# Optimization experiments

Measured on AMD Instinct MI355X. Metric: run time of the kernel, lower is better.

## Reference

```python
import jax, jax.numpy as jnp
import numpy as np

EPS = 1e-7
PROJ_EPS = 1e-5
MAX_TANH_ARG = 15.0
COMBINE_RELS_WEIGHT = 0.1


def _norm(x):
    return jnp.sqrt(jnp.sum(x * x, axis=-1, keepdims=True))


def log_map_zero(x):
    n = _norm(x)
    nc = jnp.clip(n, EPS, 1.0 - PROJ_EPS)
    return jnp.arctanh(nc) * x / jnp.maximum(n, EPS)


def exp_map_zero(v):
    n = jnp.maximum(_norm(v), EPS)
    return jnp.tanh(jnp.minimum(n, MAX_TANH_ARG)) * v / n


def hyperbolic_projection(x):
    n = jnp.maximum(_norm(x), EPS)
    maxnorm = 1.0 - PROJ_EPS
    return x * jnp.minimum(1.0, maxnorm / n)


def mobius_addition(u, v):
    uv = jnp.sum(u * v, axis=-1, keepdims=True)
    u2 = jnp.sum(u * u, axis=-1, keepdims=True)
    v2 = jnp.sum(v * v, axis=-1, keepdims=True)
    num = (1.0 + 2.0 * uv + v2) * u + (1.0 - u2) * v
    den = 1.0 + 2.0 * uv + u2 * v2
    return num / jnp.maximum(den, EPS)


def setup_inputs() -> dict:
    key = jax.random.key(0)
    ks = jax.random.split(key, 9)
    N, R, D, E = 50000, 1000, 128, 640000
    # embeddings start well inside the Poincare ball
    ents = 0.01 * jax.random.normal(ks[0], (N, D), dtype=jnp.float32)
    rels = 0.01 * jax.random.normal(ks[1], (R, D), dtype=jnp.float32)
    W_ent = jax.random.normal(ks[2], (D, D), dtype=jnp.float32) * (1.0 / np.sqrt(D))
    bias_vec = jnp.zeros((1, D), dtype=jnp.float32)
    ent_row = jax.random.randint(ks[3], (E,), 0, N, dtype=jnp.int32)
    ent_col = jax.random.randint(ks[4], (E,), 0, N, dtype=jnp.int32)
    rel_row = jax.random.randint(ks[5], (E,), 0, N, dtype=jnp.int32)
    rel_val = jax.random.randint(ks[6], (E,), 0, R, dtype=jnp.int32)
    near_rels_num = (1.0 + jax.random.randint(ks[7], (N,), 0, 32, dtype=jnp.int32)).astype(jnp.float32)
    return {"ents_embed_input": ents, "rels_embed_input": rels, "W_ent": W_ent,
            "bias_vec": bias_vec, "ent_row": ent_row, "ent_col": ent_col,
            "rel_row": rel_row, "rel_val": rel_val, "near_rels_num": near_rels_num}


def reference(ents_embed_input, rels_embed_input, W_ent, bias_vec,
              ent_row, ent_col, rel_row, rel_val, near_rels_num):
    N = ents_embed_input.shape[0]
    # tangent-space map + linear transform
    ents_tan = log_map_zero(ents_embed_input)          # [N, D]
    h = ents_tan @ W_ent                                # [N, D]
    # GAT-style sparse attention on adjacency (scores are detached in original)
    hd = jax.lax.stop_gradient(h)
    scores = jnp.sum(hd[ent_row] * hd[ent_col], axis=-1)  # [E]
    m = jax.ops.segment_max(scores, ent_row, num_segments=N)
    e = jnp.exp(scores - m[ent_row])
    denom = jax.ops.segment_sum(e, ent_row, num_segments=N)
    alpha = e / jnp.maximum(denom[ent_row], EPS)           # [E]
    near_ents = jax.ops.segment_sum(alpha[:, None] * h[ent_col], ent_row, num_segments=N)
    # relation neighborhood mean (gather + scatter-sum)
    edge_emb = rels_embed_input[rel_val]                   # [E, D]
    near_rels = jax.ops.segment_sum(edge_emb, rel_row, num_segments=N)
    near_rels = near_rels / near_rels_num[:, None]
    out = hyperbolic_projection(exp_map_zero(near_ents + COMBINE_RELS_WEIGHT * near_rels))
    b = hyperbolic_projection(exp_map_zero(bias_vec))
    out = hyperbolic_projection(mobius_addition(out, b))
    return out
```

## Files before the change

kernel.cpp:

```cpp
#include <hip/hip_runtime.h>
#include <hip/hip_fp16.h>
#include <math.h>

#define EPS 1e-7f
#define PROJ_EPS 1e-5f
#define MAXNORM (1.0f - PROJ_EPS)
#define D_DIM 128
#define CAP 48
#define PSHIFT 7
#define NPART 392
#define PCAP 2048
#define CHUNK 4096
#define NCONV 32
#define ATS 136
#define WTS 136
#define PREP_SMEM (64 * 132 * 4)
#define MID_SMEM (64 * ATS * 2 + 128 * WTS * 2 + 256)

typedef _Float16 f16;
typedef __attribute__((ext_vector_type(4))) _Float16 f16x4;
typedef __attribute__((ext_vector_type(8))) _Float16 f16x8;
typedef __attribute__((ext_vector_type(4))) float f32x4;

__device__ inline float wred(float v) {
    #pragma unroll
    for (int o = 32; o; o >>= 1) v += __shfl_xor(v, o, 64);
    return v;
}
__device__ inline float gred(float v) {
    v += __shfl_xor(v, 1, 64);
    v += __shfl_xor(v, 2, 64);
    v += __shfl_xor(v, 4, 64);
    v += __shfl_xor(v, 8, 64);
    return v;
}
__device__ inline void gred2(float& a, float& b) {
    a += __shfl_xor(a, 1, 64);  b += __shfl_xor(b, 1, 64);
    a += __shfl_xor(a, 2, 64);  b += __shfl_xor(b, 2, 64);
    a += __shfl_xor(a, 4, 64);  b += __shfl_xor(b, 4, 64);
    a += __shfl_xor(a, 8, 64);  b += __shfl_xor(b, 8, 64);
}
__device__ inline __half2 bc_h2(unsigned int u) { return *(__half2*)&u; }
__device__ inline unsigned int bc_u32(__half2 h) { return *(unsigned int*)&h; }

typedef _Float16 h2v __attribute__((ext_vector_type(2)));
__device__ inline h2v as_h2v(unsigned int u) { union { unsigned int u; h2v h; } c; c.u = u; return c.h; }

__device__ inline float dot8d(uint4 a, uint4 v) {
#if __has_builtin(__builtin_amdgcn_fdot2)
    float s = __builtin_amdgcn_fdot2(as_h2v(a.x), as_h2v(v.x), 0.f, false);
    s = __builtin_amdgcn_fdot2(as_h2v(a.y), as_h2v(v.y), s, false);
    s = __builtin_amdgcn_fdot2(as_h2v(a.z), as_h2v(v.z), s, false);
    s = __builtin_amdgcn_fdot2(as_h2v(a.w), as_h2v(v.w), s, false);
    return s;
#else
    __half2 t = __hmul2(bc_h2(a.x), bc_h2(v.x));
    t = __hfma2(bc_h2(a.y), bc_h2(v.y), t);
    t = __hfma2(bc_h2(a.z), bc_h2(v.z), t);
    t = __hfma2(bc_h2(a.w), bc_h2(v.w), t);
    return __low2float(t) + __high2float(t);
#endif
}
__device__ inline void acc8h(__half2* A, float w, uint4 v) {
    __half2 w2 = __float2half2_rn(w);
    A[0] = __hfma2(w2, bc_h2(v.x), A[0]);
    A[1] = __hfma2(w2, bc_h2(v.y), A[1]);
    A[2] = __hfma2(w2, bc_h2(v.z), A[2]);
    A[3] = __hfma2(w2, bc_h2(v.w), A[3]);
}
__device__ inline void add8h(__half2* A, uint4 v) {
    A[0] = __hadd2(A[0], bc_h2(v.x));
    A[1] = __hadd2(A[1], bc_h2(v.y));
    A[2] = __hadd2(A[2], bc_h2(v.z));
    A[3] = __hadd2(A[3], bc_h2(v.w));
}

__global__ __launch_bounds__(256) void k_prep(
    const float* __restrict__ W, f16* __restrict__ Wt_h,
    const int* __restrict__ er, const int* __restrict__ ec,
    const int* __restrict__ rr, const int* __restrict__ rv,
    int* __restrict__ part_e, int* __restrict__ part_r,
    int* __restrict__ cursors,
    const float* __restrict__ bias, float* __restrict__ bws,
    const float* __restrict__ rels, f16* __restrict__ rels_h, int relsN4,
    int E, int nChunk) {
    __shared__ alignas(16) unsigned char smem[PREP_SMEM];
    int tid = threadIdx.x;
    int bid = blockIdx.x;

    if (bid == 0) {
        if (tid < 64) {
            int l = tid;
            float2 bv = ((const float2*)bias)[l];
            float bn = fmaxf(sqrtf(wred(bv.x * bv.x + bv.y * bv.y)), EPS);
            float gb = tanhf(fminf(bn, 15.f)) / bn;
            float bx = gb * bv.x, by = gb * bv.y;
            float nb = fmaxf(sqrtf(wred(bx * bx + by * by)), EPS);
            float pb = fminf(1.f, MAXNORM / nb);
            bx *= pb; by *= pb;
            ((float2*)bws)[l] = make_float2(bx, by);
            float v2 = wred(bx * bx + by * by);
            if (l == 0) bws[128] = v2;
        }
        return;
    }

    if (bid == 1) {
        float* lts = (float*)smem;
        unsigned int* wt_u = (unsigned int*)Wt_h;
        for (int pass = 0; pass < 2; pass++) {
            #pragma unroll
            for (int i = 0; i < 8; i++) {
                int flat = (tid + i * 256) * 4;
                int kr = flat >> 7, cc = flat & 127;
                float4 x = *(const float4*)(W + (size_t)(pass * 64 + kr) * D_DIM + cc);
                *(float4*)&lts[kr * 132 + cc] = x;
            }
            __syncthreads();
            #pragma unroll
            for (int i = 0; i < 16; i++) {
                int flat2 = tid + i * 256;
                int c = flat2 >> 5, kp = flat2 & 31;
                float lo = lts[(2 * kp) * 132 + c];
                float hi = lts[(2 * kp + 1) * 132 + c];
                wt_u[c * 64 + pass * 32 + kp] = bc_u32(__float22half2_rn(make_float2(lo, hi)));
            }
            __syncthreads();
        }
        return;
    }

    if (bid < 2 + NCONV) {
        int gtid = (bid - 2) * 256 + tid;
        for (int i = gtid; i < relsN4; i += NCONV * 256) {
            float4 x = ((const float4*)rels)[i];
            uint2 u;
            u.x = bc_u32(__float22half2_rn(make_float2(x.x, x.y)));
            u.y = bc_u32(__float22half2_rn(make_float2(x.z, x.w)));
            ((uint2*)rels_h)[i] = u;
        }
        return;
    }

    int pid = bid - 2 - NCONV;
    int pair = (pid >= nChunk) ? 1 : 0;
    int chunk = pair ? pid - nChunk : pid;
    int* hist = (int*)smem;
    int* dlt  = hist + NPART;
    int* sc   = dlt + NPART;
    int* st   = sc + 256;
    const int* rsrc = pair ? rr : er;
    const int* psrc = pair ? rv : ec;
    int* part = pair ? part_r : part_e;
    int* cur  = cursors + pair * NPART;
    int e0 = chunk * CHUNK;
    int n = min(CHUNK, E - e0);

    for (int i = tid; i < NPART; i += 256) hist[i] = 0;
    __syncthreads();

    int myr[16], rk[16];
    #pragma unroll
    for (int i = 0; i < 16; i++) {
        int e = e0 + tid + i * 256;
        if (e < E) {
            int r = rsrc[e];
            myr[i] = r;
            rk[i] = atomicAdd(&hist[r >> PSHIFT], 1);
        } else myr[i] = -1;
    }
    __syncthreads();

    int h0 = (2 * tid < NPART) ? hist[2 * tid] : 0;
    int h1 = (2 * tid + 1 < NPART) ? hist[2 * tid + 1] : 0;
    int s = h0 + h1;
    sc[tid] = s;
    __syncthreads();
    for (int off = 1; off < 256; off <<= 1) {
        int v = (tid >= off) ? sc[tid - off] : 0;
        __syncthreads();
        sc[tid] += v;
        __syncthreads();
    }
    int excl = sc[tid] - s;
    if (2 * tid < NPART) dlt[2 * tid] = excl;
    if (2 * tid + 1 < NPART) dlt[2 * tid + 1] = excl + h0;
    __syncthreads();

    #pragma unroll
    for (int i = 0; i < 16; i++) {
        if (myr[i] >= 0) {
            int e = e0 + tid + i * 256;
            unsigned int pk = ((unsigned int)myr[i] << 16) | (unsigned int)(psrc[e] & 0xFFFF);
            st[dlt[myr[i] >> PSHIFT] + rk[i]] = (int)pk;
        }
    }
    __syncthreads();

    for (int p = tid; p < NPART; p += 256) {
        int len = hist[p];
        if (len > 0) {
            int g = atomicAdd(&cur[p], len);
            if (g + len > PCAP) g = PCAP - len;
            if (g < 0) g = 0;
            dlt[p] = p * PCAP + g - dlt[p];
        }
    }
    __syncthreads();

    for (int i = tid; i < n; i += 256) {
        unsigned int v = (unsigned int)st[i];
        int p = (int)(v >> 16) >> PSHIFT;
        part[dlt[p] + i] = (int)v;
    }
}

__global__ __launch_bounds__(256) void k_mid(
    const float* __restrict__ ents, const f16* __restrict__ Wt_h,
    __half* __restrict__ hh,
    const int* __restrict__ part_e, const int* __restrict__ part_r,
    const int* __restrict__ cursors,
    unsigned short* __restrict__ pay_e, unsigned short* __restrict__ pay_r,
    int* __restrict__ cnt, int N, int nGemm) {
    __shared__ alignas(16) unsigned char smem[MID_SMEM];
    int tid = threadIdx.x;
    int bid = blockIdx.x;

    if (bid < nGemm) {
        f16* atile = (f16*)smem;
        f16* wtile = (f16*)(smem + 64 * ATS * 2);
        float* fac = (float*)(smem + 64 * ATS * 2 + 128 * WTS * 2);
        int lane = tid & 63;
        int wv = tid >> 6;
        int r0 = bid * 64;

        #pragma unroll
        for (int i = 0; i < 8; i++) {
            int flat = (tid + i * 256) * 4;
            int rr2 = flat >> 7, cc = flat & 127;
            float4 x = make_float4(0.f, 0.f, 0.f, 0.f);
            if (r0 + rr2 < N) x = *(const float4*)(ents + (size_t)(r0 + rr2) * D_DIM + cc);
            f16x4 v4 = {(f16)x.x, (f16)x.y, (f16)x.z, (f16)x.w};
            *(f16x4*)&atile[rr2 * ATS + cc] = v4;
            float s = x.x * x.x + x.y * x.y + x.z * x.z + x.w * x.w;
            s += __shfl_xor(s, 1, 64);
            s += __shfl_xor(s, 2, 64);
            s += __shfl_xor(s, 4, 64);
            s += __shfl_xor(s, 8, 64);
            s += __shfl_xor(s, 16, 64);
            if ((lane & 31) == 0) fac[rr2] = s;
        }
        #pragma unroll
        for (int i = 0; i < 8; i++) {
            int flat4 = tid + i * 256;
            int c = flat4 >> 4, off = (flat4 & 15) * 8;
            uint4 u = ((const uint4*)Wt_h)[flat4];
            *(uint4*)&wtile[c * WTS + off] = u;
        }
        __syncthreads();

        if (tid < 64) {
            float n = sqrtf(fac[tid]);
            float ncl = fminf(fmaxf(n, EPS), MAXNORM);
            float at = 0.5f * logf((1.f + ncl) / (1.f - ncl));
            fac[tid] = at / fmaxf(n, EPS);
        }
        __syncthreads();

        int l15 = lane & 15, kseg = lane >> 4;
        int arow = wv * 16 + l15;

        f32x4 acc[8];
        #pragma unroll
        for (int ct = 0; ct < 8; ct++) acc[ct] = (f32x4){0.f, 0.f, 0.f, 0.f};

        #pragma unroll
        for (int ks = 0; ks < 4; ks++) {
            int k0 = ks * 32 + kseg * 8;
            f16x8 af = *(const f16x8*)&atile[arow * ATS + k0];
            #pragma unroll
            for (int ct = 0; ct < 8; ct++) {
                f16x8 bf = *(const f16x8*)&wtile[(ct * 16 + l15) * WTS + k0];
                acc[ct] = __builtin_amdgcn_mfma_f32_16x16x32_f16(af, bf, acc[ct], 0, 0, 0);
            }
        }
        __syncthreads();

        #pragma unroll
        for (int rg = 0; rg < 4; rg++) {
            int m = wv * 16 + kseg * 4 + rg;
            float fc = fac[m];
            #pragma unroll
            for (int ct = 0; ct < 8; ct++) {
                atile[m * ATS + ct * 16 + l15] = (f16)(acc[ct][rg] * fc);
            }
        }
        __syncthreads();

        #pragma unroll
        for (int i = 0; i < 4; i++) {
            int flat4 = tid + i * 256;
            int rr2 = flat4 >> 4, off = (flat4 & 15) * 8;
            if (r0 + rr2 < N) {
                uint4 u = *(const uint4*)&atile[rr2 * ATS + off];
                *(uint4*)((char*)hh + ((size_t)(r0 + rr2)) * 256 + off * 2) = u;
            }
        }
        return;
    }

    int b2 = bid - nGemm;
    int pair = (b2 >= NPART) ? 1 : 0;
    int p = pair ? b2 - NPART : b2;
    int* bcnt = (int*)smem;
    unsigned short* bb = (unsigned short*)(smem + 512);
    const int* part = (pair ? part_r : part_e) + (size_t)p * PCAP;
    unsigned short* pay = pair ? pay_r : pay_e;
    int* cnt_out = cnt + (size_t)pair * N;
    int n = min(cursors[pair * NPART + p], PCAP);

    if (tid < 128) bcnt[tid] = 0;
    __syncthreads();

    for (int i = tid; i < n; i += 256) {
        unsigned int v = (unsigned int)part[i];
        int rl = (int)((v >> 16) & 127);
        int slot = atomicAdd(&bcnt[rl], 1);
        if (slot < CAP) bb[rl * CAP + slot] = (unsigned short)(v & 0xFFFF);
    }
    __syncthreads();

    int rbase = p * 128;
    uint4* gdst = (uint4*)(pay + (size_t)rbase * CAP);
    const uint4* gsrc = (const uint4*)bb;
    for (int i = tid; i < 768; i += 256) gdst[i] = gsrc[i];
    if (tid < 128 && rbase + tid < N) cnt_out[rbase + tid] = bcnt[tid];
}

__global__ __launch_bounds__(256) void k_row(
    const __half* __restrict__ hh, const __half* __restrict__ rels_h,
    const float* __restrict__ bws, const float* __restrict__ nrn,
    const int* __restrict__ cnt, const unsigned short* __restrict__ pay_e,
    const unsigned short* __restrict__ pay_r,
    float* __restrict__ out, int N) {
    int wv = threadIdx.x >> 6, lane = threadIdx.x & 63;
    int r = blockIdx.x * 4 + wv;
    if (r >= N) return;
    int sub = lane >> 4;
    int sl = lane & 15;

    const char* hB = (const char*)hh + sl * 16;
    const char* rB = (const char*)rels_h + sl * 16;
    uint4 hraw = *(const uint4*)(hB + ((size_t)r << 8));

    int deg  = min(cnt[r], CAP);
    int degr = min(cnt[N + r], CAP);
    int myidx = (lane < deg)  ? (int)pay_e[(size_t)r * CAP + lane] : 0;
    int myrel = (lane < degr) ? (int)pay_r[(size_t)r * CAP + lane] : 0;

    __half2 aA[4] = {bc_h2(0u), bc_h2(0u), bc_h2(0u), bc_h2(0u)};
    float den = 0.f;
    int full = deg >> 2, rem = deg & 3;
    int t = 0;
    for (; t + 2 <= full; t += 2) {
        int c0 = __shfl(myidx, t * 4 + sub);
        int c1 = __shfl(myidx, t * 4 + 4 + sub);
        uint4 v0 = *(const uint4*)(hB + ((size_t)c0 << 8));
        uint4 v1 = *(const uint4*)(hB + ((size_t)c1 << 8));
        float s0 = dot8d(hraw, v0);
        float s1 = dot8d(hraw, v1);
        gred2(s0, s1);
        float w0 = __expf(s0), w1 = __expf(s1);
        den += w0 + w1;
        acc8h(aA, w0, v0);
        acc8h(aA, w1, v1);
    }
    if (t < full) {
        int c0 = __shfl(myidx, t * 4 + sub);
        uint4 v0 = *(const uint4*)(hB + ((size_t)c0 << 8));
        float s0 = gred(dot8d(hraw, v0));
        float w0 = __expf(s0);
        den += w0;
        acc8h(aA, w0, v0);
    }
    if (rem) {
        int c0 = __shfl(myidx, full * 4 + sub);
        uint4 v0 = *(const uint4*)(hB + ((size_t)c0 << 8));
        float s0 = gred(dot8d(hraw, v0));
        float w0 = (sub < rem) ? __expf(s0) : 0.f;
        den += w0;
        acc8h(aA, w0, v0);
    }

    __half2 rA[4] = {bc_h2(0u), bc_h2(0u), bc_h2(0u), bc_h2(0u)};
    int fq = degr >> 2, rq = degr & 3;
    int q = 0;
    for (; q + 2 <= fq; q += 2) {
        int i0 = __shfl(myrel, q * 4 + sub);
        int i1 = __shfl(myrel, q * 4 + 4 + sub);
        uint4 v0 = *(const uint4*)(rB + ((size_t)i0 << 8));
        uint4 v1 = *(const uint4*)(rB + ((size_t)i1 << 8));
        add8h(rA, v0);
        add8h(rA, v1);
    }
    if (q < fq) {
        int i0 = __shfl(myrel, q * 4 + sub);
        uint4 v0 = *(const uint4*)(rB + ((size_t)i0 << 8));
        add8h(rA, v0);
    }
    if (rq) {
        int i0 = __shfl(myrel, fq * 4 + sub);
        uint4 v0 = *(const uint4*)(rB + ((size_t)i0 << 8));
        if (sub < rq) add8h(rA, v0);
    }

    den += __shfl_xor(den, 16, 64);
    den += __shfl_xor(den, 32, 64);
    #pragma unroll
    for (int st2 = 16; st2 <= 32; st2 <<= 1) {
        #pragma unroll
        for (int j = 0; j < 4; j++) {
            unsigned int ua = (unsigned int)__shfl_xor((int)bc_u32(aA[j]), st2, 64);
            aA[j] = __hadd2(aA[j], bc_h2(ua));
            unsigned int ur = (unsigned int)__shfl_xor((int)bc_u32(rA[j]), st2, 64);
            rA[j] = __hadd2(rA[j], bc_h2(ur));
        }
    }

    float inv  = 1.f / fmaxf(den, EPS);
    float innr = 0.1f / nrn[r];
    float2 a0 = __half22float2(aA[0]), a1 = __half22float2(aA[1]);
    float2 a2 = __half22float2(aA[2]), a3 = __half22float2(aA[3]);
    float2 r0f = __half22float2(rA[0]), r1f = __half22float2(rA[1]);
    float2 r2f = __half22float2(rA[2]), r3f = __half22float2(rA[3]);
    float v0 = a0.x * inv + r0f.x * innr, v1 = a0.y * inv + r0f.y * innr;
    float v2_ = a1.x * inv + r1f.x * innr, v3 = a1.y * inv + r1f.y * innr;
    float v4 = a2.x * inv + r2f.x * innr, v5 = a2.y * inv + r2f.y * innr;
    float v6 = a3.x * inv + r3f.x * innr, v7 = a3.y * inv + r3f.y * innr;

    float pn = v0*v0 + v1*v1 + v2_*v2_ + v3*v3 + v4*v4 + v5*v5 + v6*v6 + v7*v7;
    pn = gred(pn);
    float sq = sqrtf(pn);
    float nn = fmaxf(sq, EPS);
    float tt = __expf(2.f * fminf(nn, 15.f));
    float g = (tt - 1.f) / ((tt + 1.f) * nn);
    float n2 = fmaxf(g * sq, EPS);
    float pf = fminf(1.f, MAXNORM / n2);
    float gp = g * pf;
    float o0 = gp*v0, o1 = gp*v1, o2 = gp*v2_, o3 = gp*v3;
    float o4 = gp*v4, o5 = gp*v5, o6 = gp*v6, o7 = gp*v7;
    float un = n2 * pf;
    float u2 = un * un;

    const float4* bp = (const float4*)(bws + sl * 8);
    float4 b0 = bp[0], b1 = bp[1];
    float bv2 = bws[128];
    float puv = o0*b0.x + o1*b0.y + o2*b0.z + o3*b0.w
              + o4*b1.x + o5*b1.y + o6*b1.z + o7*b1.w;
    puv = gred(puv);
    float ca = 1.f + 2.f * puv + bv2;
    float cb = 1.f - u2;
    float idm = 1.f / fmaxf(1.f + 2.f * puv + u2 * bv2, EPS);
    float x0 = (ca*o0 + cb*b0.x) * idm, x1 = (ca*o1 + cb*b0.y) * idm;
    float x2 = (ca*o2 + cb*b0.z) * idm, x3 = (ca*o3 + cb*b0.w) * idm;
    float x4 = (ca*o4 + cb*b1.x) * idm, x5 = (ca*o5 + cb*b1.y) * idm;
    float x6 = (ca*o6 + cb*b1.z) * idm, x7 = (ca*o7 + cb*b1.w) * idm;
    float pr = x0*x0 + x1*x1 + x2*x2 + x3*x3 + x4*x4 + x5*x5 + x6*x6 + x7*x7;
    pr = gred(pr);
    float n3 = fmaxf(sqrtf(pr), EPS);
    float pf3 = fminf(1.f, MAXNORM / n3);

    if (sub == 0) {
        float4* op = (float4*)(out + (size_t)r * D_DIM + sl * 8);
        op[0] = make_float4(x0 * pf3, x1 * pf3, x2 * pf3, x3 * pf3);
        op[1] = make_float4(x4 * pf3, x5 * pf3, x6 * pf3, x7 * pf3);
    }
}

extern "C" void kernel_launch(void* const* d_in, const int* in_sizes, int n_in,
                              void* d_out, int out_size, void* d_ws, size_t ws_size,
                              hipStream_t stream) {
    const float* ents = (const float*)d_in[0];
    const float* rels = (const float*)d_in[1];
    const float* W    = (const float*)d_in[2];
    const float* bias = (const float*)d_in[3];
    const int* er = (const int*)d_in[4];
    const int* ec = (const int*)d_in[5];
    const int* rr = (const int*)d_in[6];
    const int* rv = (const int*)d_in[7];
    const float* nrn = (const float*)d_in[8];
    int N = in_sizes[0] / D_DIM;
    int R = in_sizes[1] / D_DIM;
    int E = in_sizes[4];
    float* out = (float*)d_out;

    char* p = (char*)d_ws;
    auto alloc = [&](size_t bytes) {
        char* q = p;
        p += (bytes + 255) & ~(size_t)255;
        return q;
    };
    const int PADN = NPART * 128;
    __half* hh     = (__half*)alloc((size_t)N * D_DIM * 2);
    f16* rels_h    = (f16*)alloc((size_t)R * D_DIM * 2);
    f16* Wt_h      = (f16*)alloc((size_t)D_DIM * D_DIM * 2);
    int* cnt    = (int*)alloc((size_t)2 * N * 4);
    unsigned short* pay_e = (unsigned short*)alloc((size_t)PADN * CAP * 2);
    unsigned short* pay_r = (unsigned short*)alloc((size_t)PADN * CAP * 2);
    int* part_e = (int*)alloc((size_t)NPART * PCAP * 4);
    int* part_r = (int*)alloc((size_t)NPART * PCAP * 4);
    int* cursors = (int*)alloc((size_t)2 * NPART * 4);
    float* bws   = (float*)alloc((size_t)132 * 4);

    hipMemsetAsync(cursors, 0, (size_t)2 * NPART * 4, stream);

    int nGemm = (N + 63) / 64;
    int nChunk = (E + CHUNK - 1) / CHUNK;
    int relsN4 = R * D_DIM / 4;

    k_prep<<<2 + NCONV + 2 * nChunk, 256, 0, stream>>>(
        W, Wt_h, er, ec, rr, rv, part_e, part_r, cursors, bias, bws,
        rels, rels_h, relsN4, E, nChunk);

    k_mid<<<nGemm + 2 * NPART, 256, 0, stream>>>(
        ents, Wt_h, hh, part_e, part_r, cursors, pay_e, pay_r, cnt, N, nGemm);

    k_row<<<(N + 3) / 4, 256, 0, stream>>>(
        hh, (const __half*)rels_h, bws, nrn, cnt, pay_e, pay_r, out, N);
}
```

Before: 89.35 us.

## Map one row per 16-lane group in k_row instead of one row per wave

The row kernel now assigns each 16-lane quarter-wave its own output row, so each wave handles four rows instead of splitting one row's edges across four sub-groups. This removes the cross-subgroup shuffle reductions of accumulators and denominators and cuts the grid by four. Loops run to the wave-wide max degree, with per-row masking, so rows with smaller degree in a wave waste issue slots on divergent trip counts.

```diff
diff --git a/kernel.cpp b/kernel.cpp
--- a/kernel.cpp
+++ b/kernel.cpp
@@ -344,91 +344,110 @@
     const unsigned short* __restrict__ pay_r,
     float* __restrict__ out, int N) {
     int wv = threadIdx.x >> 6, lane = threadIdx.x & 63;
-    int r = blockIdx.x * 4 + wv;
-    if (r >= N) return;
-    int sub = lane >> 4;
-    int sl = lane & 15;
+    int sub = lane >> 4, sl = lane & 15;
+    int gb = lane & 48;
+    int r = blockIdx.x * 16 + wv * 4 + sub;
+    bool valid = r < N;
+    int rc = valid ? r : 0;
 
     const char* hB = (const char*)hh + sl * 16;
     const char* rB = (const char*)rels_h + sl * 16;
-    uint4 hraw = *(const uint4*)(hB + ((size_t)r << 8));
-
-    int deg  = min(cnt[r], CAP);
-    int degr = min(cnt[N + r], CAP);
-    int myidx = (lane < deg)  ? (int)pay_e[(size_t)r * CAP + lane] : 0;
-    int myrel = (lane < degr) ? (int)pay_r[(size_t)r * CAP + lane] : 0;
+    uint4 hraw = *(const uint4*)(hB + ((size_t)rc << 8));
+
+    int deg  = valid ? min(cnt[rc], CAP) : 0;
+    int degr = valid ? min(cnt[N + rc], CAP) : 0;
+
+    size_t be = (size_t)rc * CAP;
+    int i0e = (sl      < deg) ? (int)pay_e[be + sl]      : 0;
+    int i1e = (sl + 16 < deg) ? (int)pay_e[be + sl + 16] : 0;
+    int i2e = (sl + 32 < deg) ? (int)pay_e[be + sl + 32] : 0;
+    int i0r = (sl      < degr) ? (int)pay_r[be + sl]      : 0;
+    int i1r = (sl + 16 < degr) ? (int)pay_r[be + sl + 16] : 0;
+    int i2r = (sl + 32 < degr) ? (int)pay_r[be + sl + 32] : 0;
+
+    int md = deg;
+    md = max(md, __shfl_xor(md, 16, 64));
+    md = max(md, __shfl_xor(md, 32, 64));
+    int mdr = degr;
+    mdr = max(mdr, __shfl_xor(mdr, 16, 64));
+    mdr = max(mdr, __shfl_xor(mdr, 32, 64));
 
     __half2 aA[4] = {bc_h2(0u), bc_h2(0u), bc_h2(0u), bc_h2(0u)};
     float den = 0.f;
-    int full = deg >> 2, rem = deg & 3;
-    int t = 0;
-    for (; t + 2 <= full; t += 2) {
-        int c0 = __shfl(myidx, t * 4 + sub);
-        int c1 = __shfl(myidx, t * 4 + 4 + sub);
+
+    auto att1 = [&](int idxreg, int k, int t) {
+        int c = __shfl(idxreg, gb | k);
+        uint4 v = *(const uint4*)(hB + ((size_t)c << 8));
+        float s = gred(dot8d(hraw, v));
+        float w = (t < deg) ? __expf(s) : 0.f;
+        den += w;
+        acc8h(aA, w, v);
+    };
+    auto att2 = [&](int idxreg, int k, int t) {
+        int c0 = __shfl(idxreg, gb | k);
+        int c1 = __shfl(idxreg, gb | (k + 1));
         uint4 v0 = *(const uint4*)(hB + ((size_t)c0 << 8));
         uint4 v1 = *(const uint4*)(hB + ((size_t)c1 << 8));
         float s0 = dot8d(hraw, v0);
         float s1 = dot8d(hraw, v1);
         gred2(s0, s1);
-        float w0 = __expf(s0), w1 = __expf(s1);
+        float w0 = (t < deg) ? __expf(s0) : 0.f;
+        float w1 = (t + 1 < deg) ? __expf(s1) : 0.f;
         den += w0 + w1;
         acc8h(aA, w0, v0);
         acc8h(aA, w1, v1);
-    }
-    if (t < full) {
-        int c0 = __shfl(myidx, t * 4 + sub);
-        uint4 v0 = *(const uint4*)(hB + ((size_t)c0 << 8));
-        float s0 = gred(dot8d(hraw, v0));
-        float w0 = __expf(s0);
-        den += w0;
-        acc8h(aA, w0, v0);
-    }
-    if (rem) {
-        int c0 = __shfl(myidx, full * 4 + sub);
-        uint4 v0 = *(const uint4*)(hB + ((size_t)c0 << 8));
-        float s0 = gred(dot8d(hraw, v0));
-        float w0 = (sub < rem) ? __expf(s0) : 0.f;
-        den += w0;
-        acc8h(aA, w0, v0);
+    };
+
+    {
+        int l0 = min(md, 16);
+        int k = 0;
+        for (; k + 2 <= l0; k += 2) att2(i0e, k, k);
+        if (k < l0) att1(i0e, k, k);
+        if (md > 16) {
+            int l1 = min(md - 16, 16);
+            for (k = 0; k + 2 <= l1; k += 2) att2(i1e, k, 16 + k);
+            if (k < l1) att1(i1e, k, 16 + k);
+            if (md > 32) {
+                int l2 = min(md - 32, 16);
+                for (k = 0; k + 2 <= l2; k += 2) att2(i2e, k, 32 + k);
+                if (k < l2) att1(i2e, k, 32 + k);
+            }
+        }
     }
 
     __half2 rA[4] = {bc_h2(0u), bc_h2(0u), bc_h2(0u), bc_h2(0u)};
-    int fq = degr >> 2, rq = degr & 3;
-    int q = 0;
-    for (; q + 2 <= fq; q += 2) {
-        int i0 = __shfl(myrel, q * 4 + sub);
-        int i1 = __shfl(myrel, q * 4 + 4 + sub);
-        uint4 v0 = *(const uint4*)(rB + ((size_t)i0 << 8));
-        uint4 v1 = *(const uint4*)(rB + ((size_t)i1 << 8));
-        add8h(rA, v0);
-        add8h(rA, v1);
-    }
-    if (q < fq) {
-        int i0 = __shfl(myrel, q * 4 + sub);
-        uint4 v0 = *(const uint4*)(rB + ((size_t)i0 << 8));
-        add8h(rA, v0);
-    }
-    if (rq) {
-        int i0 = __shfl(myrel, fq * 4 + sub);
-        uint4 v0 = *(const uint4*)(rB + ((size_t)i0 << 8));
-        if (sub < rq) add8h(rA, v0);
-    }
-
-    den += __shfl_xor(den, 16, 64);
-    den += __shfl_xor(den, 32, 64);
-    #pragma unroll
-    for (int st2 = 16; st2 <= 32; st2 <<= 1) {
-        #pragma unroll
-        for (int j = 0; j < 4; j++) {
-            unsigned int ua = (unsigned int)__shfl_xor((int)bc_u32(aA[j]), st2, 64);
-            aA[j] = __hadd2(aA[j], bc_h2(ua));
-            unsigned int ur = (unsigned int)__shfl_xor((int)bc_u32(rA[j]), st2, 64);
-            rA[j] = __hadd2(rA[j], bc_h2(ur));
+    auto rel1 = [&](int idxreg, int k, int t) {
+        int id = __shfl(idxreg, gb | k);
+        uint4 v = *(const uint4*)(rB + ((size_t)id << 8));
+        if (t < degr) add8h(rA, v);
+    };
+    auto rel2 = [&](int idxreg, int k, int t) {
+        int id0 = __shfl(idxreg, gb | k);
+        int id1 = __shfl(idxreg, gb | (k + 1));
+        uint4 v0 = *(const uint4*)(rB + ((size_t)id0 << 8));
+        uint4 v1 = *(const uint4*)(rB + ((size_t)id1 << 8));
+        if (t < degr) add8h(rA, v0);
+        if (t + 1 < degr) add8h(rA, v1);
+    };
+    {
+        int l0 = min(mdr, 16);
+        int k = 0;
+        for (; k + 2 <= l0; k += 2) rel2(i0r, k, k);
+        if (k < l0) rel1(i0r, k, k);
+        if (mdr > 16) {
+            int l1 = min(mdr - 16, 16);
+            for (k = 0; k + 2 <= l1; k += 2) rel2(i1r, k, 16 + k);
+            if (k < l1) rel1(i1r, k, 16 + k);
+            if (mdr > 32) {
+                int l2 = min(mdr - 32, 16);
+                for (k = 0; k + 2 <= l2; k += 2) rel2(i2r, k, 32 + k);
+                if (k < l2) rel1(i2r, k, 32 + k);
+            }
         }
     }
 
     float inv  = 1.f / fmaxf(den, EPS);
-    float innr = 0.1f / nrn[r];
+    float innr = 0.1f / nrn[rc];
     float2 a0 = __half22float2(aA[0]), a1 = __half22float2(aA[1]);
     float2 a2 = __half22float2(aA[2]), a3 = __half22float2(aA[3]);
     float2 r0f = __half22float2(rA[0]), r1f = __half22float2(rA[1]);
@@ -470,7 +489,7 @@
     float n3 = fmaxf(sqrtf(pr), EPS);
     float pf3 = fminf(1.f, MAXNORM / n3);
 
-    if (sub == 0) {
+    if (valid) {
         float4* op = (float4*)(out + (size_t)r * D_DIM + sl * 8);
         op[0] = make_float4(x0 * pf3, x1 * pf3, x2 * pf3, x3 * pf3);
         op[1] = make_float4(x4 * pf3, x5 * pf3, x6 * pf3, x7 * pf3);
@@ -525,6 +544,6 @@
     k_mid<<<nGemm + 2 * NPART, 256, 0, stream>>>(
         ents, Wt_h, hh, part_e, part_r, cursors, pay_e, pay_r, cnt, N, nGemm);
 
-    k_row<<<(N + 3) / 4, 256, 0, stream>>>(
+    k_row<<<(N + 15) / 16, 256, 0, stream>>>(
         hh, (const __half*)rels_h, bws, nrn, cnt, pay_e, pay_r, out, N);
 }
```

After: 81.21 us. -9.1%, faster.
